# Performance work log

Hardware: AMD Instinct MI355X
Metric: run time of the kernel (lower is better)

Reference implementation:

```python
import jax, jax.numpy as jnp
import numpy as np
from jax import lax

B, CIN, COUT, H, W = 16, 128, 256, 56, 56
KH, KW = 3, 3
STRIDE = (1, 1)
PAD = ((1, 1), (1, 1))
DILATION = (1, 1)
GROUPS = 1


def setup_inputs() -> dict:
    key = jax.random.key(0)
    k1, k2, k3 = jax.random.split(key, 3)
    x = jax.random.normal(k1, (B, CIN, H, W), dtype=jnp.float32)
    weight = jax.random.normal(k2, (COUT, CIN // GROUPS, KH, KW), dtype=jnp.float32)
    bias = jax.random.normal(k3, (COUT,), dtype=jnp.float32)
    return {"x": x, "weight": weight, "bias": bias}


def reference(x, weight, bias):
    # Toeplitz matrix-vector product == grouped 2D convolution (cross-correlation)
    # with zero padding, plus per-output-channel bias.
    out = lax.conv_general_dilated(
        x, weight,
        window_strides=STRIDE,
        padding=PAD,
        rhs_dilation=DILATION,
        dimension_numbers=("NCHW", "OIHW", "NCHW"),
        feature_group_count=GROUPS,
    )
    return out + bias[None, :, None, None]
```

## Files before the change

kernel.cpp:

```cpp
#include <hip/hip_runtime.h>
#include <hip/hip_bf16.h>


#define XT_BYTES   15204352u
#define SLACK      8192u
#define WT_OFFSET  (XT_BYTES + SLACK)
#define WT_BYTES   589824u
#define WS_NEED    (WT_OFFSET + WT_BYTES)

typedef __bf16 bf16x8 __attribute__((ext_vector_type(8)));
typedef float  f32x4  __attribute__((ext_vector_type(4)));
typedef unsigned short ushort8v __attribute__((ext_vector_type(8)));

__device__ __forceinline__ unsigned short f2bf(float f) {
  unsigned u = __builtin_bit_cast(unsigned, f);
  u += 0x7fffu + ((u >> 16) & 1u);
  return (unsigned short)(u >> 16);
}

__device__ __forceinline__ void gll16(const void* g, const void* l) {
  __builtin_amdgcn_global_load_lds(
      (const __attribute__((address_space(1))) unsigned int*)g,
      (__attribute__((address_space(3))) unsigned int*)l, 16, 0, 0);
}

__global__ void prep(const float* __restrict__ x, const float* __restrict__ wsrc,
                     unsigned short* __restrict__ xt, unsigned short* __restrict__ wt) {
  int blk = blockIdx.x;
  int t = threadIdx.x;
  if (blk < 896) {
    __shared__ unsigned short tile[128][58];
    int b = blk / 56, h = blk % 56;
    int ci = t >> 1, half = t & 1;
    const float* src = x + ((size_t)(b * 128 + ci)) * 3136 + h * 56 + half * 28;
    #pragma unroll
    for (int q = 0; q < 7; ++q) {
      float4 v = *(const float4*)&src[q * 4];
      int wb = half * 28 + q * 4;
      tile[ci][wb + 0] = f2bf(v.x);
      tile[ci][wb + 1] = f2bf(v.y);
      tile[ci][wb + 2] = f2bf(v.z);
      tile[ci][wb + 3] = f2bf(v.w);
    }
    unsigned short* row = xt + (size_t)b * 475136 + (size_t)(h + 1) * 8192;
    if (t < 128) {
      int slot = t >> 4;
      int px = slot ? 56 + slot : 0;
      uint4 z; z.x = z.y = z.z = z.w = 0u;
      *(uint4*)(row + px * 128 + (t & 15) * 8) = z;
    }
    __syncthreads();
    if (t < 224) {
      int wo = t >> 2, chunk = t & 3;
      unsigned short* dst = row + (size_t)(wo + 1) * 128 + chunk * 32;
      #pragma unroll
      for (int q = 0; q < 4; ++q) {
        ushort8v v;
        #pragma unroll
        for (int j = 0; j < 8; ++j) v[j] = tile[chunk * 32 + q * 8 + j][wo];
        *(ushort8v*)&dst[q * 8] = v;
      }
    }
  } else if (blk < 928) {
    int idx = blk - 896;
    int b = idx >> 1, zr = (idx & 1) ? 57 : 0;
    uint4* dst = (uint4*)(xt + (size_t)b * 475136 + (size_t)zr * 8192);
    uint4 z; z.x = z.y = z.z = z.w = 0u;
    #pragma unroll
    for (int q = 0; q < 4; ++q) dst[t + q * 256] = z;
  } else {
    int kt = blk - 928;
    int tap = kt >> 1;
    int ci0 = (kt & 1) * 64;
    #pragma unroll
    for (int q = 0; q < 8; ++q) {
      int n = t + q * 256;
      int co = n >> 3;
      int kg = (n & 7) ^ (co & 7);
      const float* src = wsrc + (size_t)co * 1152 + (size_t)(ci0 + kg * 8) * 9 + tap;
      ushort8v v;
      #pragma unroll
      for (int j = 0; j < 8; ++j) v[j] = f2bf(src[j * 9]);
      *(ushort8v*)&wt[(size_t)kt * 16384 + n * 8] = v;
    }
  }
}


__global__ __launch_bounds__(512, 2) void conv_gemm(
    const unsigned short* __restrict__ xt,
    const char* __restrict__ wt,
    const float* __restrict__ bias,
    float* __restrict__ out) {
  __shared__ __align__(16) char lds[131072];

  int bid = blockIdx.x;
  int sw = (bid & 7) * 28 + (bid >> 3);
  int bimg = sw / 14;
  int h0 = (sw - bimg * 14) * 4;

  int tid = threadIdx.x;
  int wv = tid >> 6, l = tid & 63;
  int wm = wv >> 2, wn = wv & 3;
  int lm = l & 15, lg = l >> 4, x7 = lm & 7;

  int aoff0 = wm * 16384 + lm * 128 + ((lg ^ x7) << 4);
  int boff0 = 32768 + wn * 8192 + lm * 128 + ((lg ^ x7) << 4);

  const char* aB = wt + wv * 4096 + l * 16;
  const unsigned short* bB[4];
  #pragma unroll
  for (int q = 0; q < 4; ++q) {
    int n = wv * 256 + q * 64 + l;
    int px = n >> 3;
    int kg = (n & 7) ^ (px & 7);
    bB[q] = xt + ((size_t)((bimg * 58 + h0 + (px >> 6)) * 64 + (px & 63))) * 128 + kg * 8;
  }

  f32x4 acc[8][4];
  #pragma unroll
  for (int m = 0; m < 8; ++m)
    #pragma unroll
    for (int n = 0; n < 4; ++n)
      acc[m][n] = (f32x4){0.f, 0.f, 0.f, 0.f};

  auto stage = [&](int kt, int buf) {
    int tap = kt >> 1;
    int kh = tap >= 6 ? 2 : (tap >= 3 ? 1 : 0);
    int kw = tap - kh * 3;
    int koff = (kh * 64 + kw) * 128 + (kt & 1) * 64;
    char* dA = &lds[buf * 65536 + wv * 4096];
    char* dB = &lds[buf * 65536 + 32768 + wv * 4096];
    const char* sA = aB + kt * 32768;
    #pragma unroll
    for (int q = 0; q < 4; ++q) {
      gll16(sA + q * 1024, dA + q * 1024);
      gll16(bB[q] + koff, dB + q * 1024);
    }
  };

  stage(0, 0);
  __syncthreads();

  for (int kt = 0; kt < 18; ++kt) {
    const char* base = &lds[(kt & 1) * 65536];
    if (kt < 17) stage(kt + 1, (kt + 1) & 1);
    bf16x8 a0[8], b0[4];
    #pragma unroll
    for (int m = 0; m < 8; ++m) a0[m] = *(const bf16x8*)(base + aoff0 + m * 2048);
    #pragma unroll
    for (int n = 0; n < 4; ++n) b0[n] = *(const bf16x8*)(base + boff0 + n * 2048);
    __builtin_amdgcn_s_setprio(1);
    #pragma unroll
    for (int m = 0; m < 8; ++m)
      #pragma unroll
      for (int n = 0; n < 4; ++n)
        acc[m][n] = __builtin_amdgcn_mfma_f32_16x16x32_bf16(a0[m], b0[n], acc[m][n], 0, 0, 0);
    __builtin_amdgcn_s_setprio(0);
    bf16x8 a1[8], b1[4];
    #pragma unroll
    for (int m = 0; m < 8; ++m) a1[m] = *(const bf16x8*)(base + ((aoff0 ^ 64) + m * 2048));
    #pragma unroll
    for (int n = 0; n < 4; ++n) b1[n] = *(const bf16x8*)(base + ((boff0 ^ 64) + n * 2048));
    __builtin_amdgcn_s_setprio(1);
    #pragma unroll
    for (int m = 0; m < 8; ++m)
      #pragma unroll
      for (int n = 0; n < 4; ++n)
        acc[m][n] = __builtin_amdgcn_mfma_f32_16x16x32_bf16(a1[m], b1[n], acc[m][n], 0, 0, 0);
    __builtin_amdgcn_s_setprio(0);
    if (kt < 17) __syncthreads();
  }

  #pragma unroll
  for (int m = 0; m < 8; ++m) {
    int co = wm * 128 + m * 16 + lg * 4;
    f32x4 bb = *(const f32x4*)&bias[co];
    size_t obase = ((size_t)bimg * 256 + co) * 3136;
    #pragma unroll
    for (int n = 0; n < 4; ++n) {
      int px = wn * 64 + n * 16 + lm;
      int w_ = px & 63;
      int h_ = h0 + (px >> 6);
      if (w_ < 56) {
        float* o = out + obase + (size_t)h_ * 56 + w_;
        #pragma unroll
        for (int r = 0; r < 4; ++r)
          o[(size_t)r * 3136] = acc[m][n][r] + bb[r];
      }
    }
  }
}


__global__ void conv_naive(const float* __restrict__ x, const float* __restrict__ w,
                           const float* __restrict__ bias, float* __restrict__ out) {
  int idx = blockIdx.x * 256 + threadIdx.x;
  if (idx >= 16 * 256 * 56 * 56) return;
  int wo = idx % 56; int t = idx / 56;
  int ho = t % 56; t /= 56;
  int co = t % 256; int b = t / 256;
  float acc = bias[co];
  for (int ci = 0; ci < 128; ++ci) {
    const float* xp = x + ((size_t)(b * 128 + ci)) * 3136;
    const float* wp = w + ((size_t)(co * 128 + ci)) * 9;
    for (int kh = 0; kh < 3; ++kh) {
      int hi = ho + kh - 1;
      if (hi < 0 || hi >= 56) continue;
      for (int kw = 0; kw < 3; ++kw) {
        int wi = wo + kw - 1;
        if (wi < 0 || wi >= 56) continue;
        acc += xp[hi * 56 + wi] * wp[kh * 3 + kw];
      }
    }
  }
  out[idx] = acc;
}

extern "C" void kernel_launch(void* const* d_in, const int* in_sizes, int n_in,
                              void* d_out, int out_size, void* d_ws, size_t ws_size,
                              hipStream_t stream) {
  const float* x    = (const float*)d_in[0];
  const float* wgt  = (const float*)d_in[1];
  const float* bias = (const float*)d_in[2];
  float* out = (float*)d_out;

  if (ws_size < (size_t)WS_NEED) {
    conv_naive<<<(16 * 256 * 56 * 56 + 255) / 256, 256, 0, stream>>>(x, wgt, bias, out);
    return;
  }

  unsigned short* xt = (unsigned short*)d_ws;
  unsigned short* wt = (unsigned short*)((char*)d_ws + WT_OFFSET);

  prep<<<946, 256, 0, stream>>>(x, wgt, xt, wt);
  conv_gemm<<<224, 512, 0, stream>>>(xt, (const char*)wt, bias, out);
}
```

Baseline: 57.78 us.

## Split K-tile into four phases with interleaved staging and explicit barriers

Restructures the conv GEMM main loop so each K-tile is processed in four sub-phases, each issuing a slice of the next tile's global-to-LDS loads between LDS fragment reads and MFMA bursts. Synchronisation moves from __syncthreads to explicit s_barrier, sched_barrier and partial vmcnt waits. The weight and activation LDS layouts change to an unswizzled K-half-split form, with the prep kernel rewritten to match. The aim is finer overlap of memory traffic with MFMA work and fewer live fragment registers. The cost is many more barriers per iteration and possible LDS bank conflicts, since the XOR swizzle is gone.

```diff
diff --git a/kernel.cpp b/kernel.cpp
--- a/kernel.cpp
+++ b/kernel.cpp
@@ -11,6 +11,10 @@
 typedef __bf16 bf16x8 __attribute__((ext_vector_type(8)));
 typedef float  f32x4  __attribute__((ext_vector_type(4)));
 typedef unsigned short ushort8v __attribute__((ext_vector_type(8)));
+
+#define BAR()  __builtin_amdgcn_s_barrier()
+#define SB0()  __builtin_amdgcn_sched_barrier(0)
+#define LGKM0() asm volatile("s_waitcnt lgkmcnt(0)" ::: "memory")
 
 __device__ __forceinline__ unsigned short f2bf(float f) {
   unsigned u = __builtin_bit_cast(unsigned, f);
@@ -71,17 +75,18 @@
   } else {
     int kt = blk - 928;
     int tap = kt >> 1;
-    int ci0 = (kt & 1) * 64;
-    #pragma unroll
-    for (int q = 0; q < 8; ++q) {
-      int n = t + q * 256;
-      int co = n >> 3;
-      int kg = (n & 7) ^ (co & 7);
-      const float* src = wsrc + (size_t)co * 1152 + (size_t)(ci0 + kg * 8) * 9 + tap;
-      ushort8v v;
-      #pragma unroll
-      for (int j = 0; j < 8; ++j) v[j] = f2bf(src[j * 9]);
-      *(ushort8v*)&wt[(size_t)kt * 16384 + n * 8] = v;
+    int ci_base = (kt & 1) * 64;
+    int co = t;
+    #pragma unroll
+    for (int khh = 0; khh < 2; ++khh) {
+      const float* src = wsrc + (size_t)co * 1152 + (size_t)(ci_base + khh * 32) * 9 + tap;
+      #pragma unroll
+      for (int g = 0; g < 4; ++g) {
+        ushort8v v;
+        #pragma unroll
+        for (int j = 0; j < 8; ++j) v[j] = f2bf(src[(g * 8 + j) * 9]);
+        *(ushort8v*)&wt[(size_t)kt * 16384 + khh * 8192 + co * 32 + g * 8] = v;
+      }
     }
   }
 }
@@ -89,7 +94,7 @@
 
 __global__ __launch_bounds__(512, 2) void conv_gemm(
     const unsigned short* __restrict__ xt,
-    const char* __restrict__ wt,
+    const char* __restrict__ wtb,
     const float* __restrict__ bias,
     float* __restrict__ out) {
   __shared__ __align__(16) char lds[131072];
@@ -102,20 +107,18 @@
   int tid = threadIdx.x;
   int wv = tid >> 6, l = tid & 63;
   int wm = wv >> 2, wn = wv & 3;
-  int lm = l & 15, lg = l >> 4, x7 = lm & 7;
-
-  int aoff0 = wm * 16384 + lm * 128 + ((lg ^ x7) << 4);
-  int boff0 = 32768 + wn * 8192 + lm * 128 + ((lg ^ x7) << 4);
-
-  const char* aB = wt + wv * 4096 + l * 16;
-  const unsigned short* bB[4];
-  #pragma unroll
-  for (int q = 0; q < 4; ++q) {
-    int n = wv * 256 + q * 64 + l;
-    int px = n >> 3;
-    int kg = (n & 7) ^ (px & 7);
-    bB[q] = xt + ((size_t)((bimg * 58 + h0 + (px >> 6)) * 64 + (px & 63))) * 128 + kg * 8;
-  }
+  int lm = l & 15, lg = l >> 4;
+
+  int aRd = (wm * 128 + lm) * 64 + lg * 16;
+  int bRd = 32768 + (wn * 64 + lm) * 64 + lg * 16;
+
+  const char* aS = wtb + tid * 16;
+  int px0 = tid >> 2, q = tid & 3;
+  const unsigned short* bS0 = xt +
+      ((size_t)((bimg * 58 + h0 + (px0 >> 6)) * 64 + (px0 & 63))) * 128 + q * 8;
+  int px1 = 128 + px0;
+  const unsigned short* bS1 = xt +
+      ((size_t)((bimg * 58 + h0 + (px1 >> 6)) * 64 + (px1 & 63))) * 128 + q * 8;
 
   f32x4 acc[8][4];
   #pragma unroll
@@ -124,52 +127,93 @@
     for (int n = 0; n < 4; ++n)
       acc[m][n] = (f32x4){0.f, 0.f, 0.f, 0.f};
 
-  auto stage = [&](int kt, int buf) {
+  auto stageA = [&](int kt, int khh, char* nb) {
+    const char* s = aS + kt * 32768 + khh * 16384;
+    char* d = nb + khh * 16384 + tid * 16;
+    gll16(s, d);
+    gll16(s + 8192, d + 8192);
+  };
+  auto stageB = [&](int kt, int khh, char* nb) {
     int tap = kt >> 1;
-    int kh = tap >= 6 ? 2 : (tap >= 3 ? 1 : 0);
-    int kw = tap - kh * 3;
-    int koff = (kh * 64 + kw) * 128 + (kt & 1) * 64;
-    char* dA = &lds[buf * 65536 + wv * 4096];
-    char* dB = &lds[buf * 65536 + 32768 + wv * 4096];
-    const char* sA = aB + kt * 32768;
-    #pragma unroll
-    for (int q = 0; q < 4; ++q) {
-      gll16(sA + q * 1024, dA + q * 1024);
-      gll16(bB[q] + koff, dB + q * 1024);
-    }
+    int kh_t = tap >= 6 ? 2 : (tap >= 3 ? 1 : 0);
+    int kw_t = tap - 3 * kh_t;
+    int koff = (kh_t * 64 + kw_t) * 128 + (kt & 1) * 64 + khh * 32;
+    char* d = nb + 32768 + khh * 16384 + tid * 16;
+    gll16(bS0 + koff, d);
+    gll16(bS1 + koff, d + 8192);
   };
 
-  stage(0, 0);
-  __syncthreads();
+  {
+    char* b0 = &lds[0];
+    stageA(0, 0, b0); stageB(0, 0, b0);
+    stageA(0, 1, b0); stageB(0, 1, b0);
+  }
+  asm volatile("s_waitcnt vmcnt(4)" ::: "memory");
+  SB0(); BAR(); SB0();
 
   for (int kt = 0; kt < 18; ++kt) {
     const char* base = &lds[(kt & 1) * 65536];
-    if (kt < 17) stage(kt + 1, (kt + 1) & 1);
-    bf16x8 a0[8], b0[4];
-    #pragma unroll
-    for (int m = 0; m < 8; ++m) a0[m] = *(const bf16x8*)(base + aoff0 + m * 2048);
-    #pragma unroll
-    for (int n = 0; n < 4; ++n) b0[n] = *(const bf16x8*)(base + boff0 + n * 2048);
-    __builtin_amdgcn_s_setprio(1);
-    #pragma unroll
-    for (int m = 0; m < 8; ++m)
-      #pragma unroll
-      for (int n = 0; n < 4; ++n)
-        acc[m][n] = __builtin_amdgcn_mfma_f32_16x16x32_bf16(a0[m], b0[n], acc[m][n], 0, 0, 0);
-    __builtin_amdgcn_s_setprio(0);
-    bf16x8 a1[8], b1[4];
-    #pragma unroll
-    for (int m = 0; m < 8; ++m) a1[m] = *(const bf16x8*)(base + ((aoff0 ^ 64) + m * 2048));
-    #pragma unroll
-    for (int n = 0; n < 4; ++n) b1[n] = *(const bf16x8*)(base + ((boff0 ^ 64) + n * 2048));
-    __builtin_amdgcn_s_setprio(1);
-    #pragma unroll
-    for (int m = 0; m < 8; ++m)
-      #pragma unroll
-      for (int n = 0; n < 4; ++n)
-        acc[m][n] = __builtin_amdgcn_mfma_f32_16x16x32_bf16(a1[m], b1[n], acc[m][n], 0, 0, 0);
-    __builtin_amdgcn_s_setprio(0);
-    if (kt < 17) __syncthreads();
+    char* nbase = &lds[((kt & 1) ^ 1) * 65536];
+    bf16x8 a[4], bb[4];
+
+    #pragma unroll
+    for (int m = 0; m < 4; ++m) a[m] = *(const bf16x8*)(base + aRd + m * 1024);
+    #pragma unroll
+    for (int n = 0; n < 4; ++n) bb[n] = *(const bf16x8*)(base + bRd + n * 1024);
+    if (kt < 17) stageA(kt + 1, 0, nbase);
+    SB0(); BAR(); LGKM0(); SB0();
+    __builtin_amdgcn_s_setprio(1);
+    #pragma unroll
+    for (int m = 0; m < 4; ++m)
+      #pragma unroll
+      for (int n = 0; n < 4; ++n)
+        acc[m][n] = __builtin_amdgcn_mfma_f32_16x16x32_bf16(a[m], bb[n], acc[m][n], 0, 0, 0);
+    __builtin_amdgcn_s_setprio(0);
+    SB0(); BAR(); SB0();
+
+    #pragma unroll
+    for (int m = 0; m < 4; ++m) a[m] = *(const bf16x8*)(base + aRd + 4096 + m * 1024);
+    if (kt < 17) stageB(kt + 1, 0, nbase);
+    SB0(); BAR(); LGKM0(); SB0();
+    __builtin_amdgcn_s_setprio(1);
+    #pragma unroll
+    for (int m = 0; m < 4; ++m)
+      #pragma unroll
+      for (int n = 0; n < 4; ++n)
+        acc[m + 4][n] = __builtin_amdgcn_mfma_f32_16x16x32_bf16(a[m], bb[n], acc[m + 4][n], 0, 0, 0);
+    __builtin_amdgcn_s_setprio(0);
+    if (kt < 17) asm volatile("s_waitcnt vmcnt(4)" ::: "memory");
+    else         asm volatile("s_waitcnt vmcnt(0)" ::: "memory");
+    SB0(); BAR(); SB0();
+
+    #pragma unroll
+    for (int m = 0; m < 4; ++m) a[m] = *(const bf16x8*)(base + 16384 + aRd + m * 1024);
+    #pragma unroll
+    for (int n = 0; n < 4; ++n) bb[n] = *(const bf16x8*)(base + 16384 + bRd + n * 1024);
+    if (kt < 17) stageA(kt + 1, 1, nbase);
+    SB0(); BAR(); LGKM0(); SB0();
+    __builtin_amdgcn_s_setprio(1);
+    #pragma unroll
+    for (int m = 0; m < 4; ++m)
+      #pragma unroll
+      for (int n = 0; n < 4; ++n)
+        acc[m][n] = __builtin_amdgcn_mfma_f32_16x16x32_bf16(a[m], bb[n], acc[m][n], 0, 0, 0);
+    __builtin_amdgcn_s_setprio(0);
+    SB0(); BAR(); SB0();
+
+    #pragma unroll
+    for (int m = 0; m < 4; ++m) a[m] = *(const bf16x8*)(base + 16384 + aRd + 4096 + m * 1024);
+    if (kt < 17) stageB(kt + 1, 1, nbase);
+    SB0(); BAR(); LGKM0(); SB0();
+    __builtin_amdgcn_s_setprio(1);
+    #pragma unroll
+    for (int m = 0; m < 4; ++m)
+      #pragma unroll
+      for (int n = 0; n < 4; ++n)
+        acc[m + 4][n] = __builtin_amdgcn_mfma_f32_16x16x32_bf16(a[m], bb[n], acc[m + 4][n], 0, 0, 0);
+    __builtin_amdgcn_s_setprio(0);
+    if (kt < 17) asm volatile("s_waitcnt vmcnt(4)" ::: "memory");
+    SB0(); BAR(); SB0();
   }
 
   #pragma unroll
```

New measurement: 65.53 us. 1.13x slower.

## Restructure conv GEMM main loop into barrier-phased pipeline with prefetch distance two

Applied to the files above, without the earlier changes.

Splits the main loop into four MFMA phases separated by explicit workgroup barriers and manual lgkmcnt/vmcnt waits. The A and B global-to-LDS loads for iteration kt+2 are issued into the buffer currently being read, interleaved between MFMA phases. The goal is to hide load latency better and to keep waves in lockstep so LDS reads overlap MFMA work. In exchange it adds many more barriers per iteration, and reusing the current buffer depends on careful wait ordering, which risks races or stalls.

```diff
diff --git a/kernel.cpp b/kernel.cpp
--- a/kernel.cpp
+++ b/kernel.cpp
@@ -11,6 +11,10 @@
 typedef __bf16 bf16x8 __attribute__((ext_vector_type(8)));
 typedef float  f32x4  __attribute__((ext_vector_type(4)));
 typedef unsigned short ushort8v __attribute__((ext_vector_type(8)));
+
+#define BAR()   __builtin_amdgcn_s_barrier()
+#define SB0()   __builtin_amdgcn_sched_barrier(0)
+#define LGKM0() asm volatile("s_waitcnt lgkmcnt(0)" ::: "memory")
 
 __device__ __forceinline__ unsigned short f2bf(float f) {
   unsigned u = __builtin_bit_cast(unsigned, f);
@@ -124,52 +128,84 @@
     for (int n = 0; n < 4; ++n)
       acc[m][n] = (f32x4){0.f, 0.f, 0.f, 0.f};
 
-  auto stage = [&](int kt, int buf) {
+  auto stageA = [&](int kt, int buf) {
+    const char* sA = aB + kt * 32768;
+    char* dA = &lds[buf * 65536 + wv * 4096];
+    #pragma unroll
+    for (int q = 0; q < 4; ++q) gll16(sA + q * 1024, dA + q * 1024);
+  };
+  auto stageB = [&](int kt, int buf) {
     int tap = kt >> 1;
     int kh = tap >= 6 ? 2 : (tap >= 3 ? 1 : 0);
     int kw = tap - kh * 3;
     int koff = (kh * 64 + kw) * 128 + (kt & 1) * 64;
-    char* dA = &lds[buf * 65536 + wv * 4096];
     char* dB = &lds[buf * 65536 + 32768 + wv * 4096];
-    const char* sA = aB + kt * 32768;
-    #pragma unroll
-    for (int q = 0; q < 4; ++q) {
-      gll16(sA + q * 1024, dA + q * 1024);
-      gll16(bB[q] + koff, dB + q * 1024);
-    }
+    #pragma unroll
+    for (int q = 0; q < 4; ++q) gll16(bB[q] + koff, dB + q * 1024);
   };
 
-  stage(0, 0);
-  __syncthreads();
+  stageA(0, 0); stageB(0, 0);
+  stageA(1, 1); stageB(1, 1);
+  asm volatile("s_waitcnt vmcnt(8)" ::: "memory");
+  SB0(); BAR(); SB0();
 
   for (int kt = 0; kt < 18; ++kt) {
     const char* base = &lds[(kt & 1) * 65536];
-    if (kt < 17) stage(kt + 1, (kt + 1) & 1);
-    bf16x8 a0[8], b0[4];
+    int cur = kt & 1;
+    bf16x8 a0[8], a1[8], bb0[4], bb1[4];
+
     #pragma unroll
     for (int m = 0; m < 8; ++m) a0[m] = *(const bf16x8*)(base + aoff0 + m * 2048);
     #pragma unroll
-    for (int n = 0; n < 4; ++n) b0[n] = *(const bf16x8*)(base + boff0 + n * 2048);
-    __builtin_amdgcn_s_setprio(1);
-    #pragma unroll
-    for (int m = 0; m < 8; ++m)
-      #pragma unroll
-      for (int n = 0; n < 4; ++n)
-        acc[m][n] = __builtin_amdgcn_mfma_f32_16x16x32_bf16(a0[m], b0[n], acc[m][n], 0, 0, 0);
-    __builtin_amdgcn_s_setprio(0);
-    bf16x8 a1[8], b1[4];
+    for (int n = 0; n < 4; ++n) bb0[n] = *(const bf16x8*)(base + boff0 + n * 2048);
+    SB0(); BAR(); LGKM0(); SB0();
+    __builtin_amdgcn_s_setprio(1);
+    #pragma unroll
+    for (int m = 0; m < 4; ++m)
+      #pragma unroll
+      for (int n = 0; n < 4; ++n)
+        acc[m][n] = __builtin_amdgcn_mfma_f32_16x16x32_bf16(a0[m], bb0[n], acc[m][n], 0, 0, 0);
+    __builtin_amdgcn_s_setprio(0);
+    SB0(); BAR(); SB0();
+
     #pragma unroll
     for (int m = 0; m < 8; ++m) a1[m] = *(const bf16x8*)(base + ((aoff0 ^ 64) + m * 2048));
-    #pragma unroll
-    for (int n = 0; n < 4; ++n) b1[n] = *(const bf16x8*)(base + ((boff0 ^ 64) + n * 2048));
-    __builtin_amdgcn_s_setprio(1);
-    #pragma unroll
-    for (int m = 0; m < 8; ++m)
-      #pragma unroll
-      for (int n = 0; n < 4; ++n)
-        acc[m][n] = __builtin_amdgcn_mfma_f32_16x16x32_bf16(a1[m], b1[n], acc[m][n], 0, 0, 0);
-    __builtin_amdgcn_s_setprio(0);
-    if (kt < 17) __syncthreads();
+    SB0(); BAR(); SB0();
+    __builtin_amdgcn_s_setprio(1);
+    #pragma unroll
+    for (int m = 0; m < 4; ++m)
+      #pragma unroll
+      for (int n = 0; n < 4; ++n)
+        acc[m + 4][n] = __builtin_amdgcn_mfma_f32_16x16x32_bf16(a0[m + 4], bb0[n], acc[m + 4][n], 0, 0, 0);
+    __builtin_amdgcn_s_setprio(0);
+    LGKM0();
+    SB0(); BAR(); SB0();
+
+    #pragma unroll
+    for (int n = 0; n < 4; ++n) bb1[n] = *(const bf16x8*)(base + ((boff0 ^ 64) + n * 2048));
+    if (kt < 16) stageA(kt + 2, cur);
+    SB0(); BAR(); LGKM0(); SB0();
+    __builtin_amdgcn_s_setprio(1);
+    #pragma unroll
+    for (int m = 0; m < 4; ++m)
+      #pragma unroll
+      for (int n = 0; n < 4; ++n)
+        acc[m][n] = __builtin_amdgcn_mfma_f32_16x16x32_bf16(a1[m], bb1[n], acc[m][n], 0, 0, 0);
+    __builtin_amdgcn_s_setprio(0);
+    SB0(); BAR(); SB0();
+
+    if (kt < 16) stageB(kt + 2, cur);
+    SB0(); BAR(); SB0();
+    __builtin_amdgcn_s_setprio(1);
+    #pragma unroll
+    for (int m = 0; m < 4; ++m)
+      #pragma unroll
+      for (int n = 0; n < 4; ++n)
+        acc[m + 4][n] = __builtin_amdgcn_mfma_f32_16x16x32_bf16(a1[m + 4], bb1[n], acc[m + 4][n], 0, 0, 0);
+    __builtin_amdgcn_s_setprio(0);
+    if (kt < 16)       asm volatile("s_waitcnt vmcnt(8)" ::: "memory");
+    else if (kt == 16) asm volatile("s_waitcnt vmcnt(0)" ::: "memory");
+    SB0(); BAR(); SB0();
   }
 
   #pragma unroll
```

New measurement: 63.49 us. 9.9% more time.
